# Performance work log

Measured on AMD Instinct MI355X. Metric: run time of the kernel, lower is better.

## Reference

```python
import jax, jax.numpy as jnp
import numpy as np

N, E, FDIM, H = 50000, 1_600_000, 256, 128


def setup_inputs() -> dict:
    key = jax.random.key(0)
    ks = jax.random.split(key, 16)
    s = 0.05
    return {
        "node_features": jax.random.normal(ks[0], (N, FDIM), dtype=jnp.float32),
        "edge_index": jax.random.randint(ks[1], (2, E), 0, N, dtype=jnp.int64),
        # node encoder: Linear(F,H) -> ReLU -> Linear(H,H)
        "enc_w1": jax.random.normal(ks[2], (FDIM, H), dtype=jnp.float32) * s,
        "enc_b1": jnp.zeros((H,), dtype=jnp.float32),
        "enc_w2": jax.random.normal(ks[3], (H, H), dtype=jnp.float32) * s,
        "enc_b2": jnp.zeros((H,), dtype=jnp.float32),
        # three GCNConv layers (weight + bias each)
        "conv_w1": jax.random.normal(ks[4], (H, H), dtype=jnp.float32) * s,
        "conv_b1": jnp.zeros((H,), dtype=jnp.float32),
        "conv_w2": jax.random.normal(ks[5], (H, H), dtype=jnp.float32) * s,
        "conv_b2": jnp.zeros((H,), dtype=jnp.float32),
        "conv_w3": jax.random.normal(ks[6], (H, H), dtype=jnp.float32) * s,
        "conv_b3": jnp.zeros((H,), dtype=jnp.float32),
        # edge classifier: Linear(2H,H) -> ReLU -> Dropout(eval: identity) -> Linear(H,1) -> Sigmoid
        "cls_w1": jax.random.normal(ks[7], (2 * H, H), dtype=jnp.float32) * s,
        "cls_b1": jnp.zeros((H,), dtype=jnp.float32),
        "cls_w2": jax.random.normal(ks[8], (H, 1), dtype=jnp.float32) * s,
        "cls_b2": jnp.zeros((1,), dtype=jnp.float32),
    }


def _gcn_conv(x, w, b, src, dst, norm, n):
    # GCNConv: x' = scatter_add_dst(norm * (x W)[src]) + b  (self-loops already in src/dst/norm)
    xw = x @ w
    out = jax.ops.segment_sum(xw[src] * norm[:, None], dst, num_segments=n)
    return out + b


def reference(node_features, edge_index, enc_w1, enc_b1, enc_w2, enc_b2,
              conv_w1, conv_b1, conv_w2, conv_b2, conv_w3, conv_b3,
              cls_w1, cls_b1, cls_w2, cls_b2):
    n = node_features.shape[0]
    loops = jnp.arange(n, dtype=edge_index.dtype)
    src = jnp.concatenate([edge_index[0], loops])  # (E+N,)
    dst = jnp.concatenate([edge_index[1], loops])
    # symmetric normalization with self-loops (PyG gcn_norm defaults)
    deg = jax.ops.segment_sum(jnp.ones(src.shape, node_features.dtype), dst, num_segments=n)
    dis = jnp.where(deg > 0, jax.lax.rsqrt(jnp.maximum(deg, 1.0)), 0.0)
    norm = dis[src] * dis[dst]  # (E+N,)

    # node encoder
    x = jax.nn.relu(node_features @ enc_w1 + enc_b1) @ enc_w2 + enc_b2
    # stacked GCN layers
    x = jax.nn.relu(_gcn_conv(x, conv_w1, conv_b1, src, dst, norm, n))
    x = jax.nn.relu(_gcn_conv(x, conv_w2, conv_b2, src, dst, norm, n))
    x = _gcn_conv(x, conv_w3, conv_b3, src, dst, norm, n)

    # edge features: gather + concat  -> (E, 2H)
    ef = jnp.concatenate([x[edge_index[0]], x[edge_index[1]]], axis=1)
    h = jax.nn.relu(ef @ cls_w1 + cls_b1)  # Dropout is identity at eval
    scores = jax.nn.sigmoid(h @ cls_w2 + cls_b2)
    return scores.squeeze(-1)  # (E,)
```

## Files before the change

### kernel.cpp

```cpp
#include <hip/hip_runtime.h>
#include <math.h>

#define HDIM 128
#define BSH 7
#define MAXBUCK 512

typedef __attribute__((ext_vector_type(8))) short    bf16x8;
typedef __attribute__((ext_vector_type(4))) float    f32x4;
typedef __attribute__((ext_vector_type(2))) float    f32x2;
typedef __attribute__((ext_vector_type(8))) unsigned short u16x8;
typedef __attribute__((ext_vector_type(4))) unsigned short u16x4;
typedef __attribute__((ext_vector_type(2))) __fp16 f16x2;

__device__ __forceinline__ float bf2f(unsigned short u) {
    union { unsigned int i; float f; } c; c.i = ((unsigned int)u) << 16; return c.f;
}
__device__ __forceinline__ unsigned short f2bf(float f) {
    union { float f; unsigned int i; } c; c.f = f;
    unsigned int r = (c.i + 0x7fffu + ((c.i >> 16) & 1u)) >> 16;
    return (unsigned short)r;
}
__device__ __forceinline__ void f8x8_decp(uint2 v, f32x2* p) {
    p[0] = __builtin_amdgcn_cvt_pk_f32_fp8((int)v.x, false);
    p[1] = __builtin_amdgcn_cvt_pk_f32_fp8((int)v.x, true);
    p[2] = __builtin_amdgcn_cvt_pk_f32_fp8((int)v.y, false);
    p[3] = __builtin_amdgcn_cvt_pk_f32_fp8((int)v.y, true);
}
__device__ __forceinline__ void f8x16_dech(uint4 v, f16x2* h) {
    f32x2 p[8];
    p[0] = __builtin_amdgcn_cvt_pk_f32_fp8((int)v.x, false);
    p[1] = __builtin_amdgcn_cvt_pk_f32_fp8((int)v.x, true);
    p[2] = __builtin_amdgcn_cvt_pk_f32_fp8((int)v.y, false);
    p[3] = __builtin_amdgcn_cvt_pk_f32_fp8((int)v.y, true);
    p[4] = __builtin_amdgcn_cvt_pk_f32_fp8((int)v.z, false);
    p[5] = __builtin_amdgcn_cvt_pk_f32_fp8((int)v.z, true);
    p[6] = __builtin_amdgcn_cvt_pk_f32_fp8((int)v.w, false);
    p[7] = __builtin_amdgcn_cvt_pk_f32_fp8((int)v.w, true);
#pragma unroll
    for (int i = 0; i < 8; i++) h[i] = __builtin_amdgcn_cvt_pkrtz(p[i].x, p[i].y);
}
__device__ __forceinline__ f16x2 pkmax0(f16x2 a) {
    f16x2 r;
    asm("v_pk_max_f16 %0, %1, 0" : "=v"(r) : "v"(a));
    return r;
}
__device__ __forceinline__ float edot16(uint4 pv, const f16x2 (&qh)[8], const f16x2 (&wh)[8]) {
    f16x2 ph[8]; f8x16_dech(pv, ph);
    float acc = 0.f;
#pragma unroll
    for (int i = 0; i < 8; i++)
        acc = __builtin_amdgcn_fdot2(pkmax0(ph[i] + qh[i]), wh[i], acc, false);
    return acc;
}
__device__ __forceinline__ float fsigmoid(float x) {
    float e = __builtin_amdgcn_exp2f(-x * 1.44269504f);
    return __builtin_amdgcn_rcpf(1.f + e);
}

__global__ __launch_bounds__(256) void k_hist(
    const int* __restrict__ dst, int* __restrict__ tot,
    int* __restrict__ hist, int E, int chunk, int nbuck)
{
    __shared__ int h[MAXBUCK];
    for (int i = threadIdx.x; i < MAXBUCK; i += 256) h[i] = 0;
    __syncthreads();
    int beg = blockIdx.x * chunk;
    int fin = min(beg + chunk, E);
    for (int e = beg + threadIdx.x; e < fin; e += 256)
        atomicAdd(&h[dst[e] >> BSH], 1);
    __syncthreads();
    for (int k = threadIdx.x; k < nbuck; k += 256) {
        int v = h[k];
        hist[(size_t)blockIdx.x * nbuck + k] = v;
        if (v) atomicAdd(&tot[k], v);
    }
}

__global__ __launch_bounds__(256) void k_scan_buckets(
    const int* __restrict__ tot, int* __restrict__ gcur, int* __restrict__ base, int nbuck,
    const float* __restrict__ w2src, unsigned short* __restrict__ w2h)
{
    __shared__ int a[MAXBUCK], b[MAXBUCK];
    int t = threadIdx.x;
    if (t < 128) w2h[t] = __builtin_bit_cast(unsigned short, (__fp16)w2src[t]);
    for (int i = t; i < MAXBUCK; i += 256) a[i] = (i < nbuck) ? tot[i] : 0;
    __syncthreads();
    int* s1 = a; int* s2 = b;
    for (int off = 1; off < MAXBUCK; off <<= 1) {
        for (int i = t; i < MAXBUCK; i += 256)
            s2[i] = s1[i] + ((i >= off) ? s1[i - off] : 0);
        __syncthreads();
        int* tmp = s1; s1 = s2; s2 = tmp;
    }
    for (int i = t; i < nbuck; i += 256) {
        int e = (i == 0) ? 0 : s1[i - 1];
        gcur[i] = e;
        base[i] = e;
    }
    if (t == 0) base[nbuck] = s1[nbuck - 1];
}

__global__ __launch_bounds__(256) void k_partition(
    const int* __restrict__ src, const int* __restrict__ dst,
    const int* __restrict__ hist, int* __restrict__ gcur,
    uint2* __restrict__ stag, int E, int chunk, int nbuck)
{
    __shared__ int h[MAXBUCK];
    int t = threadIdx.x;
    for (int k = t; k < nbuck; k += 256) {
        int v = hist[(size_t)blockIdx.x * nbuck + k];
        h[k] = v ? atomicAdd(&gcur[k], v) : 0;
    }
    __syncthreads();
    int beg = blockIdx.x * chunk;
    int fin = min(beg + chunk, E);
    for (int e = beg + t; e < fin; e += 256) {
        unsigned int d = (unsigned int)dst[e];
        unsigned int s = (unsigned int)src[e];
        int pos = atomicAdd(&h[d >> BSH], 1);
        stag[pos] = make_uint2(s | (d << 16), (unsigned int)e);
    }
}

__global__ __launch_bounds__(256) void k_bucket_csr(
    const int* __restrict__ base, const uint2* __restrict__ stag,
    int* __restrict__ row_ptr, int* __restrict__ col, uint2* __restrict__ epk,
    float* __restrict__ dis, int n, int nbuck)
{
    __shared__ int cl[128], sa[128], sb[128], cur[128];
    int k = blockIdx.x;
    int n0 = k << BSH;
    int t = threadIdx.x;
    if (t < 128) cl[t] = 0;
    __syncthreads();
    int b0 = base[k];
    int m = base[k + 1] - b0;
    const uint2* seg = stag + b0;
    for (int i = t; i < m; i += 256) atomicAdd(&cl[(seg[i].x >> 16) & 127], 1);
    __syncthreads();
    int cv = 0;
    if (t < 128) { cv = cl[t]; sa[t] = cv; }
    __syncthreads();
    int* s1 = sa; int* s2 = sb;
    for (int off = 1; off < 128; off <<= 1) {
        if (t < 128) s2[t] = s1[t] + ((t >= off) ? s1[t - off] : 0);
        __syncthreads();
        int* tmp = s1; s1 = s2; s2 = tmp;
    }
    if (t < 128) {
        int node = n0 + t;
        if (node < n) {
            int rpv = b0 + s1[t] - cv;
            row_ptr[node] = rpv;
            cur[t] = rpv;
            dis[node] = rsqrtf(1.0f + (float)cv);
        }
    }
    if (k == 0 && t == 0) row_ptr[n] = base[nbuck];
    __syncthreads();
    for (int i = t; i < m; i += 256) {
        uint2 e = seg[i];
        int pos = atomicAdd(&cur[(e.x >> 16) & 127], 1);
        int s = (int)(e.x & 0xffffu);
        col[pos] = s;
        epk[pos] = make_uint2((unsigned int)s, e.y);
    }
}

struct WEnt { const float* src; unsigned short* dst; int K; };
struct WAll { WEnt w[7]; };

__global__ __launch_bounds__(256) void k_prep_w(WAll all) {
    WEnt e = all.w[blockIdx.y];
    int i = blockIdx.x * 256 + threadIdx.x;
    if (i >= e.K * HDIM) return;
    int k = i >> 7, c = i & 127;
    e.dst[(size_t)c * e.K + k] = f2bf(e.src[i]);
}

__global__ __launch_bounds__(256) void k_gemm_b(
    const unsigned short* __restrict__ X, const unsigned short* __restrict__ Wt,
    const float* __restrict__ bias, const float* __restrict__ scale,
    void* __restrict__ C, int M, int relu_out, int out_mode)
{
    __shared__ unsigned short sW[128 * 128];
    const int t = threadIdx.x;
#pragma unroll
    for (int i = 0; i < 8; i++) {
        int c = t + i * 256;
        int row = c >> 4, o = c & 15;
        int mt = row >> 4, r = row & 15, kc = o >> 2, q = o & 3;
        int lidx = (mt * 4 + kc) * 64 + q * 16 + r;
        *(uint4*)(sW + (size_t)lidx * 8) = *(const uint4*)(Wt + (size_t)c * 8);
    }
    __syncthreads();
    int wave = t >> 6, lane = t & 63;
    int quad = lane >> 4, r = lane & 15;
    int row0 = blockIdx.x * 64 + wave * 16;
    if (row0 >= M) return;
    const unsigned short* xp = X + (size_t)(row0 + r) * 128 + quad * 8;
    f32x4 acc[8];
#pragma unroll
    for (int mt = 0; mt < 8; mt++) acc[mt] = (f32x4){0.f, 0.f, 0.f, 0.f};
#pragma unroll
    for (int kc = 0; kc < 4; kc++) {
        bf16x8 xf = *(const bf16x8*)(xp + kc * 32);
#pragma unroll
        for (int mt = 0; mt < 8; mt++) {
            bf16x8 wf = *(const bf16x8*)(sW + ((size_t)((mt * 4 + kc) * 64 + lane)) * 8);
            acc[mt] = __builtin_amdgcn_mfma_f32_16x16x32_bf16(wf, xf, acc[mt], 0, 0, 0);
        }
    }
    float sc = scale ? scale[row0 + r] : 1.f;
    if (out_mode == 1) {
        unsigned char* cp = (unsigned char*)C + (size_t)(row0 + r) * HDIM + quad * 4;
#pragma unroll
        for (int mt = 0; mt < 8; mt++) {
            float v[4];
#pragma unroll
            for (int j = 0; j < 4; j++) {
                float x = acc[mt][j];
                if (bias) x += bias[mt * 16 + quad * 4 + j];
                if (relu_out) x = fmaxf(x, 0.f);
                v[j] = x * sc;
            }
            int wd = 0;
            wd = __builtin_amdgcn_cvt_pk_fp8_f32(v[0], v[1], wd, false);
            wd = __builtin_amdgcn_cvt_pk_fp8_f32(v[2], v[3], wd, true);
            *(unsigned int*)(cp + mt * 16) = (unsigned int)wd;
        }
    } else {
        unsigned short* cp = (unsigned short*)C + (size_t)(row0 + r) * HDIM + quad * 4;
#pragma unroll
        for (int mt = 0; mt < 8; mt++) {
            u16x4 o;
#pragma unroll
            for (int j = 0; j < 4; j++) {
                float v = acc[mt][j];
                if (bias) v += bias[mt * 16 + quad * 4 + j];
                if (relu_out) v = fmaxf(v, 0.f);
                o[j] = f2bf(v * sc);
            }
            *(u16x4*)(cp + mt * 16) = o;
        }
    }
}

__global__ __launch_bounds__(256) void k_gemm_nf(
    const float* __restrict__ X, const unsigned short* __restrict__ Wt,
    const float* __restrict__ bias, unsigned short* __restrict__ C,
    int M, int relu_out)
{
    const int K = 256;
    __shared__ unsigned short sW[128 * 256];
    const int t = threadIdx.x;
#pragma unroll
    for (int i = 0; i < 16; i++) {
        int c = t + i * 256;
        int row = c >> 5, o = c & 31;
        int mt = row >> 4, r = row & 15, kc = o >> 2, q = o & 3;
        int lidx = (mt * 8 + kc) * 64 + q * 16 + r;
        *(uint4*)(sW + (size_t)lidx * 8) = *(const uint4*)(Wt + (size_t)c * 8);
    }
    __syncthreads();
    int wave = t >> 6, lane = t & 63;
    int quad = lane >> 4, r = lane & 15;
    int row0 = blockIdx.x * 64 + wave * 16;
    if (row0 >= M) return;
    const float* xp = X + (size_t)(row0 + r) * K + quad * 8;
    f32x4 acc[8];
#pragma unroll
    for (int mt = 0; mt < 8; mt++) acc[mt] = (f32x4){0.f, 0.f, 0.f, 0.f};
#pragma unroll 2
    for (int kc = 0; kc < 8; kc++) {
        float4 xa = *(const float4*)(xp + kc * 32);
        float4 xb = *(const float4*)(xp + kc * 32 + 4);
        bf16x8 xf;
        xf[0] = (short)f2bf(xa.x); xf[1] = (short)f2bf(xa.y);
        xf[2] = (short)f2bf(xa.z); xf[3] = (short)f2bf(xa.w);
        xf[4] = (short)f2bf(xb.x); xf[5] = (short)f2bf(xb.y);
        xf[6] = (short)f2bf(xb.z); xf[7] = (short)f2bf(xb.w);
#pragma unroll
        for (int mt = 0; mt < 8; mt++) {
            bf16x8 wf = *(const bf16x8*)(sW + ((size_t)((mt * 8 + kc) * 64 + lane)) * 8);
            acc[mt] = __builtin_amdgcn_mfma_f32_16x16x32_bf16(wf, xf, acc[mt], 0, 0, 0);
        }
    }
    unsigned short* cp = C + (size_t)(row0 + r) * HDIM + quad * 4;
#pragma unroll
    for (int mt = 0; mt < 8; mt++) {
        u16x4 o;
#pragma unroll
        for (int j = 0; j < 4; j++) {
            float v = acc[mt][j];
            if (bias) v += bias[mt * 16 + quad * 4 + j];
            if (relu_out) v = fmaxf(v, 0.f);
            o[j] = f2bf(v);
        }
        *(u16x4*)(cp + mt * 16) = o;
    }
}

__global__ __launch_bounds__(256) void k_aggregate_f8(
    const int* __restrict__ row_ptr, const int* __restrict__ col,
    const float* __restrict__ dis, const uint2* __restrict__ y8,
    const float* __restrict__ bias, unsigned short* __restrict__ out, int n, int relu_out)
{
    int wid = (blockIdx.x * 256 + threadIdx.x) >> 6;
    if (wid >= n) return;
    int lane = threadIdx.x & 63;
    int q = lane >> 4, t = lane & 15;
    f32x2 acc[4];
    {
        uint2 sv = y8[(size_t)wid * 16 + t];
        f32x2 p[4]; f8x8_decp(sv, p);
#pragma unroll
        for (int i = 0; i < 4; i++) acc[i] = (q == 0) ? p[i] : (f32x2){0.f, 0.f};
    }
    int beg = row_ptr[wid], end = row_ptr[wid + 1];
    int j = beg + q;
    for (; j + 28 < end; j += 32) {
        int s[8];
        uint2 v[8];
#pragma unroll
        for (int u = 0; u < 8; u++) s[u] = col[j + u * 4];
#pragma unroll
        for (int u = 0; u < 8; u++) v[u] = y8[(size_t)s[u] * 16 + t];
#pragma unroll
        for (int u = 0; u < 8; u++) {
            f32x2 p[4]; f8x8_decp(v[u], p);
#pragma unroll
            for (int i = 0; i < 4; i++) acc[i] += p[i];
        }
    }
    for (; j + 12 < end; j += 16) {
        int s0 = col[j], s1 = col[j + 4], s2 = col[j + 8], s3 = col[j + 12];
        uint2 v0 = y8[(size_t)s0 * 16 + t];
        uint2 v1 = y8[(size_t)s1 * 16 + t];
        uint2 v2 = y8[(size_t)s2 * 16 + t];
        uint2 v3 = y8[(size_t)s3 * 16 + t];
        f32x2 p0[4], p1[4], p2[4], p3[4];
        f8x8_decp(v0, p0); f8x8_decp(v1, p1); f8x8_decp(v2, p2); f8x8_decp(v3, p3);
#pragma unroll
        for (int i = 0; i < 4; i++) acc[i] += (p0[i] + p1[i]) + (p2[i] + p3[i]);
    }
    for (; j < end; j += 4) {
        int s = col[j];
        uint2 v = y8[(size_t)s * 16 + t];
        f32x2 p[4]; f8x8_decp(v, p);
#pragma unroll
        for (int i = 0; i < 4; i++) acc[i] += p[i];
    }
#pragma unroll
    for (int i = 0; i < 4; i++) {
        acc[i].x += __shfl_xor(acc[i].x, 16, 64);
        acc[i].y += __shfl_xor(acc[i].y, 16, 64);
        acc[i].x += __shfl_xor(acc[i].x, 32, 64);
        acc[i].y += __shfl_xor(acc[i].y, 32, 64);
    }
    if (q == 0) {
        float di = dis[wid];
        u16x8 o;
#pragma unroll
        for (int i = 0; i < 4; i++) {
            float v0 = di * acc[i].x + bias[t * 8 + i * 2];
            float v1 = di * acc[i].y + bias[t * 8 + i * 2 + 1];
            if (relu_out) { v0 = fmaxf(v0, 0.f); v1 = fmaxf(v1, 0.f); }
            o[i * 2]     = f2bf(v0);
            o[i * 2 + 1] = f2bf(v1);
        }
        *(u16x8*)(out + (size_t)wid * HDIM + t * 8) = o;
    }
}

__global__ __launch_bounds__(256) void k_edge_score_csr(
    const int* __restrict__ row_ptr, const uint2* __restrict__ epk,
    const uint4* __restrict__ P8, const uint4* __restrict__ Q8,
    const unsigned short* __restrict__ w2h, const float* __restrict__ b2,
    float* __restrict__ out, int n)
{
    int wid = (blockIdx.x * 256 + threadIdx.x) >> 6;
    if (wid >= n) return;
    int lane = threadIdx.x & 63;
    unsigned g = (unsigned)(lane >> 3), t = (unsigned)(lane & 7);
    f16x2 wh[8], qh[8];
    {
        uint4 wv0 = *(const uint4*)(w2h + t * 16);
        uint4 wv1 = *(const uint4*)(w2h + t * 16 + 8);
        wh[0] = __builtin_bit_cast(f16x2, wv0.x);
        wh[1] = __builtin_bit_cast(f16x2, wv0.y);
        wh[2] = __builtin_bit_cast(f16x2, wv0.z);
        wh[3] = __builtin_bit_cast(f16x2, wv0.w);
        wh[4] = __builtin_bit_cast(f16x2, wv1.x);
        wh[5] = __builtin_bit_cast(f16x2, wv1.y);
        wh[6] = __builtin_bit_cast(f16x2, wv1.z);
        wh[7] = __builtin_bit_cast(f16x2, wv1.w);
        uint4 qv = Q8[(unsigned)wid * 8u + t];
        f8x16_dech(qv, qh);
    }
    float bb = b2[0];
    int beg = row_ptr[wid], end = row_ptr[wid + 1];
    int j = beg + (int)g;
    for (; j + 8 < end; j += 16) {
        uint2 e0 = epk[j], e1 = epk[j + 8];
        uint4 p0 = P8[e0.x * 8u + t];
        uint4 p1 = P8[e1.x * 8u + t];
        float s0 = edot16(p0, qh, wh);
        float s1 = edot16(p1, qh, wh);
        s0 += __shfl_xor(s0, 4, 8); s1 += __shfl_xor(s1, 4, 8);
        s0 += __shfl_xor(s0, 2, 8); s1 += __shfl_xor(s1, 2, 8);
        s0 += __shfl_xor(s0, 1, 8); s1 += __shfl_xor(s1, 1, 8);
        float sv = (t == 0) ? s0 : s1;
        unsigned eid = (t == 0) ? e0.y : e1.y;
        if (t < 2)
            __builtin_nontemporal_store(fsigmoid(sv + bb), &out[eid]);
    }
    if (j < end) {
        uint2 e0 = epk[j];
        uint4 p0 = P8[e0.x * 8u + t];
        float s0 = edot16(p0, qh, wh);
        s0 += __shfl_xor(s0, 4, 8);
        s0 += __shfl_xor(s0, 2, 8);
        s0 += __shfl_xor(s0, 1, 8);
        if (t == 0)
            __builtin_nontemporal_store(fsigmoid(s0 + bb), &out[e0.y]);
    }
}

extern "C" void kernel_launch(void* const* d_in, const int* in_sizes, int n_in,
                              void* d_out, int out_size, void* d_ws, size_t ws_size,
                              hipStream_t stream) {
    const float* nf   = (const float*)d_in[0];
    const int*   ei   = (const int*)d_in[1];
    const float* ew1  = (const float*)d_in[2];
    const float* eb1  = (const float*)d_in[3];
    const float* ew2  = (const float*)d_in[4];
    const float* eb2  = (const float*)d_in[5];
    const float* cw1  = (const float*)d_in[6];
    const float* cb1  = (const float*)d_in[7];
    const float* cw2  = (const float*)d_in[8];
    const float* cb2  = (const float*)d_in[9];
    const float* cw3  = (const float*)d_in[10];
    const float* cb3  = (const float*)d_in[11];
    const float* clw1 = (const float*)d_in[12];
    const float* clb1 = (const float*)d_in[13];
    const float* clw2 = (const float*)d_in[14];
    const float* clb2 = (const float*)d_in[15];
    float* out = (float*)d_out;

    const int FD = 256;
    const int N = in_sizes[0] / FD;
    const int E = in_sizes[1] / 2;
    const int NBUCK = (N + 127) >> BSH;
    const int PBLK = 256;
    const int chunk = (E + PBLK - 1) / PBLK;

    size_t Np = ((size_t)N + 256) & ~(size_t)255;
    char* w = (char*)d_ws;
    float* dis     = (float*)w;            w += Np * 4;
    int*   tot     = (int*)w;              w += MAXBUCK * 4;
    int*   gcur    = (int*)w;              w += MAXBUCK * 4;
    int*   base    = (int*)w;              w += (MAXBUCK + 4) * 4;
    int*   hist    = (int*)w;              w += (size_t)PBLK * MAXBUCK * 4;
    int*   row_ptr = (int*)w;              w += Np * 4;
    uint2* stag    = (uint2*)w;            w += (size_t)E * 8;
    uint2* epk     = (uint2*)w;            w += (size_t)E * 8;
    int*   col     = (int*)w;              w += (((size_t)E * 4) + 255) & ~(size_t)255;
    unsigned short* bufA = (unsigned short*)w;  w += (size_t)N * HDIM * 2;
    unsigned short* bufB = (unsigned short*)w;  w += (size_t)N * HDIM * 2;
    unsigned short* bufC = (unsigned short*)w;  w += (size_t)N * HDIM * 2;
    unsigned char*  f8X  = (unsigned char*)w;   w += ((size_t)N * HDIM + 255) & ~(size_t)255;
    unsigned char*  f8P  = (unsigned char*)w;   w += ((size_t)N * HDIM + 255) & ~(size_t)255;
    unsigned char*  f8Q  = (unsigned char*)w;   w += ((size_t)N * HDIM + 255) & ~(size_t)255;
    unsigned short* wtE1 = (unsigned short*)w;  w += 256 * HDIM * 2;
    unsigned short* wtE2 = (unsigned short*)w;  w += 128 * HDIM * 2;
    unsigned short* wtC1 = (unsigned short*)w;  w += 128 * HDIM * 2;
    unsigned short* wtC2 = (unsigned short*)w;  w += 128 * HDIM * 2;
    unsigned short* wtC3 = (unsigned short*)w;  w += 128 * HDIM * 2;
    unsigned short* wtT  = (unsigned short*)w;  w += 128 * HDIM * 2;
    unsigned short* wtB  = (unsigned short*)w;  w += 128 * HDIM * 2;
    unsigned short* w2h  = (unsigned short*)w;  w += 256 * 2;

    int gemm_grid = (N + 63) / 64;
    int ag = (N + 3) / 4;

    WAll wa;
    wa.w[0] = { ew1,               wtE1, 256 };
    wa.w[1] = { ew2,               wtE2, 128 };
    wa.w[2] = { cw1,               wtC1, 128 };
    wa.w[3] = { cw2,               wtC2, 128 };
    wa.w[4] = { cw3,               wtC3, 128 };
    wa.w[5] = { clw1,              wtT,  128 };
    wa.w[6] = { clw1 + 128 * HDIM, wtB,  128 };
    k_prep_w<<<dim3(128, 7), 256, 0, stream>>>(wa);

    hipMemsetAsync(tot, 0, MAXBUCK * sizeof(int), stream);
    k_hist<<<PBLK, 256, 0, stream>>>(ei + E, tot, hist, E, chunk, NBUCK);
    k_scan_buckets<<<1, 256, 0, stream>>>(tot, gcur, base, NBUCK, clw2, w2h);
    k_partition<<<PBLK, 256, 0, stream>>>(ei, ei + E, hist, gcur, stag, E, chunk, NBUCK);
    k_bucket_csr<<<NBUCK, 256, 0, stream>>>(base, stag, row_ptr, col, epk, dis, N, NBUCK);

    k_gemm_nf<<<gemm_grid, 256, 0, stream>>>(nf, wtE1, eb1, bufA, N, 1);
    k_gemm_b<<<gemm_grid, 256, 0, stream>>>(bufA, wtE2, eb2, nullptr, bufB, N, 0, 0);

    k_gemm_b<<<gemm_grid, 256, 0, stream>>>(bufB, wtC1, nullptr, dis, f8X, N, 0, 1);
    k_aggregate_f8<<<ag, 256, 0, stream>>>(row_ptr, col, dis, (const uint2*)f8X, cb1, bufC, N, 1);
    k_gemm_b<<<gemm_grid, 256, 0, stream>>>(bufC, wtC2, nullptr, dis, f8X, N, 0, 1);
    k_aggregate_f8<<<ag, 256, 0, stream>>>(row_ptr, col, dis, (const uint2*)f8X, cb2, bufA, N, 1);
    k_gemm_b<<<gemm_grid, 256, 0, stream>>>(bufA, wtC3, nullptr, dis, f8X, N, 0, 1);
    k_aggregate_f8<<<ag, 256, 0, stream>>>(row_ptr, col, dis, (const uint2*)f8X, cb3, bufB, N, 0);

    k_gemm_b<<<gemm_grid, 256, 0, stream>>>(bufB, wtT, clb1, nullptr, f8P, N, 0, 1);
    k_gemm_b<<<gemm_grid, 256, 0, stream>>>(bufB, wtB, nullptr, nullptr, f8Q, N, 0, 1);

    k_edge_score_csr<<<ag, 256, 0, stream>>>(row_ptr, epk, (const uint4*)f8P, (const uint4*)f8Q,
                                             w2h, clb2, out, N);
}
```

Measured before the change: 446.9 us.

## Fold encoder second linear into first conv weight; fuse P/Q GEMMs; nontemporal index loads

Precomputes We2·Wc1 and be2·Wc1 on device so the encoder's second linear layer and the first GCN projection run as one GEMM, removing one full N×H pass. The two classifier projection GEMMs are merged into one kernel that reads the input tile once and writes both fp8 outputs. Column and edge index loads in the aggregation and edge-scoring kernels become nontemporal to reduce cache pollution. The fold changes rounding, since the product is formed in fp32 and then stored in bf16, and the fused kernel uses twice the LDS per block.

```diff
diff --git a/kernel.cpp b/kernel.cpp
--- a/kernel.cpp
+++ b/kernel.cpp
@@ -56,6 +56,10 @@
     float e = __builtin_amdgcn_exp2f(-x * 1.44269504f);
     return __builtin_amdgcn_rcpf(1.f + e);
 }
+__device__ __forceinline__ uint2 nt_load_u2(const uint2* p) {
+    unsigned long long v = __builtin_nontemporal_load((const unsigned long long*)p);
+    return make_uint2((unsigned)v, (unsigned)(v >> 32));
+}
 
 __global__ __launch_bounds__(256) void k_hist(
     const int* __restrict__ dst, int* __restrict__ tot,
@@ -168,7 +172,7 @@
 }
 
 struct WEnt { const float* src; unsigned short* dst; int K; };
-struct WAll { WEnt w[7]; };
+struct WAll { WEnt w[5]; };
 
 __global__ __launch_bounds__(256) void k_prep_w(WAll all) {
     WEnt e = all.w[blockIdx.y];
@@ -176,6 +180,24 @@
     if (i >= e.K * HDIM) return;
     int k = i >> 7, c = i & 127;
     e.dst[(size_t)c * e.K + k] = f2bf(e.src[i]);
+}
+
+__global__ __launch_bounds__(256) void k_fold(
+    const float* __restrict__ We2, const float* __restrict__ be2,
+    const float* __restrict__ Wc1, unsigned short* __restrict__ WtF,
+    float* __restrict__ bF)
+{
+    int i = blockIdx.x * 256 + threadIdx.x;
+    int c = i >> 7, k = i & 127;
+    float s = 0.f;
+    for (int j = 0; j < 128; j++)
+        s += We2[k * 128 + j] * Wc1[j * 128 + c];
+    WtF[(size_t)c * 128 + k] = f2bf(s);
+    if (i < 128) {
+        float b = 0.f;
+        for (int j = 0; j < 128; j++) b += be2[j] * Wc1[j * 128 + i];
+        bF[i] = b;
+    }
 }
 
 __global__ __launch_bounds__(256) void k_gemm_b(
@@ -246,6 +268,63 @@
     }
 }
 
+__global__ __launch_bounds__(256) void k_gemm_pq(
+    const unsigned short* __restrict__ X, const unsigned short* __restrict__ WtP,
+    const unsigned short* __restrict__ WtQ, const float* __restrict__ biasP,
+    unsigned char* __restrict__ P, unsigned char* __restrict__ Q, int M)
+{
+    __shared__ unsigned short sW[2 * 128 * 128];
+    const int t = threadIdx.x;
+#pragma unroll
+    for (int i = 0; i < 8; i++) {
+        int c = t + i * 256;
+        int row = c >> 4, o = c & 15;
+        int mt = row >> 4, r = row & 15, kc = o >> 2, q = o & 3;
+        int lidx = (mt * 4 + kc) * 64 + q * 16 + r;
+        *(uint4*)(sW + (size_t)lidx * 8)         = *(const uint4*)(WtP + (size_t)c * 8);
+        *(uint4*)(sW + 16384 + (size_t)lidx * 8) = *(const uint4*)(WtQ + (size_t)c * 8);
+    }
+    __syncthreads();
+    int wave = t >> 6, lane = t & 63;
+    int quad = lane >> 4, r = lane & 15;
+    int row0 = blockIdx.x * 64 + wave * 16;
+    if (row0 >= M) return;
+    const unsigned short* xp = X + (size_t)(row0 + r) * 128 + quad * 8;
+    f32x4 accP[8], accQ[8];
+#pragma unroll
+    for (int mt = 0; mt < 8; mt++) {
+        accP[mt] = (f32x4){0.f, 0.f, 0.f, 0.f};
+        accQ[mt] = (f32x4){0.f, 0.f, 0.f, 0.f};
+    }
+#pragma unroll
+    for (int kc = 0; kc < 4; kc++) {
+        bf16x8 xf = *(const bf16x8*)(xp + kc * 32);
+#pragma unroll
+        for (int mt = 0; mt < 8; mt++) {
+            bf16x8 wfp = *(const bf16x8*)(sW + ((size_t)((mt * 4 + kc) * 64 + lane)) * 8);
+            bf16x8 wfq = *(const bf16x8*)(sW + 16384 + ((size_t)((mt * 4 + kc) * 64 + lane)) * 8);
+            accP[mt] = __builtin_amdgcn_mfma_f32_16x16x32_bf16(wfp, xf, accP[mt], 0, 0, 0);
+            accQ[mt] = __builtin_amdgcn_mfma_f32_16x16x32_bf16(wfq, xf, accQ[mt], 0, 0, 0);
+        }
+    }
+    unsigned char* pp = P + (size_t)(row0 + r) * HDIM + quad * 4;
+    unsigned char* qp = Q + (size_t)(row0 + r) * HDIM + quad * 4;
+#pragma unroll
+    for (int mt = 0; mt < 8; mt++) {
+        int wdp = 0, wdq = 0;
+        float p0 = accP[mt][0] + biasP[mt * 16 + quad * 4 + 0];
+        float p1 = accP[mt][1] + biasP[mt * 16 + quad * 4 + 1];
+        float p2 = accP[mt][2] + biasP[mt * 16 + quad * 4 + 2];
+        float p3 = accP[mt][3] + biasP[mt * 16 + quad * 4 + 3];
+        wdp = __builtin_amdgcn_cvt_pk_fp8_f32(p0, p1, wdp, false);
+        wdp = __builtin_amdgcn_cvt_pk_fp8_f32(p2, p3, wdp, true);
+        wdq = __builtin_amdgcn_cvt_pk_fp8_f32(accQ[mt][0], accQ[mt][1], wdq, false);
+        wdq = __builtin_amdgcn_cvt_pk_fp8_f32(accQ[mt][2], accQ[mt][3], wdq, true);
+        *(unsigned int*)(pp + mt * 16) = (unsigned int)wdp;
+        *(unsigned int*)(qp + mt * 16) = (unsigned int)wdq;
+    }
+}
+
 __global__ __launch_bounds__(256) void k_gemm_nf(
     const float* __restrict__ X, const unsigned short* __restrict__ Wt,
     const float* __restrict__ bias, unsigned short* __restrict__ C,
@@ -323,7 +402,7 @@
         int s[8];
         uint2 v[8];
 #pragma unroll
-        for (int u = 0; u < 8; u++) s[u] = col[j + u * 4];
+        for (int u = 0; u < 8; u++) s[u] = __builtin_nontemporal_load(&col[j + u * 4]);
 #pragma unroll
         for (int u = 0; u < 8; u++) v[u] = y8[(size_t)s[u] * 16 + t];
 #pragma unroll
@@ -334,7 +413,10 @@
         }
     }
     for (; j + 12 < end; j += 16) {
-        int s0 = col[j], s1 = col[j + 4], s2 = col[j + 8], s3 = col[j + 12];
+        int s0 = __builtin_nontemporal_load(&col[j]);
+        int s1 = __builtin_nontemporal_load(&col[j + 4]);
+        int s2 = __builtin_nontemporal_load(&col[j + 8]);
+        int s3 = __builtin_nontemporal_load(&col[j + 12]);
         uint2 v0 = y8[(size_t)s0 * 16 + t];
         uint2 v1 = y8[(size_t)s1 * 16 + t];
         uint2 v2 = y8[(size_t)s2 * 16 + t];
@@ -345,7 +427,7 @@
         for (int i = 0; i < 4; i++) acc[i] += (p0[i] + p1[i]) + (p2[i] + p3[i]);
     }
     for (; j < end; j += 4) {
-        int s = col[j];
+        int s = __builtin_nontemporal_load(&col[j]);
         uint2 v = y8[(size_t)s * 16 + t];
         f32x2 p[4]; f8x8_decp(v, p);
 #pragma unroll
@@ -402,7 +484,8 @@
     int beg = row_ptr[wid], end = row_ptr[wid + 1];
     int j = beg + (int)g;
     for (; j + 8 < end; j += 16) {
-        uint2 e0 = epk[j], e1 = epk[j + 8];
+        uint2 e0 = nt_load_u2(&epk[j]);
+        uint2 e1 = nt_load_u2(&epk[j + 8]);
         uint4 p0 = P8[e0.x * 8u + t];
         uint4 p1 = P8[e1.x * 8u + t];
         float s0 = edot16(p0, qh, wh);
@@ -416,7 +499,7 @@
             __builtin_nontemporal_store(fsigmoid(sv + bb), &out[eid]);
     }
     if (j < end) {
-        uint2 e0 = epk[j];
+        uint2 e0 = nt_load_u2(&epk[j]);
         uint4 p0 = P8[e0.x * 8u + t];
         float s0 = edot16(p0, qh, wh);
         s0 += __shfl_xor(s0, 4, 8);
@@ -473,26 +556,25 @@
     unsigned char*  f8P  = (unsigned char*)w;   w += ((size_t)N * HDIM + 255) & ~(size_t)255;
     unsigned char*  f8Q  = (unsigned char*)w;   w += ((size_t)N * HDIM + 255) & ~(size_t)255;
     unsigned short* wtE1 = (unsigned short*)w;  w += 256 * HDIM * 2;
-    unsigned short* wtE2 = (unsigned short*)w;  w += 128 * HDIM * 2;
-    unsigned short* wtC1 = (unsigned short*)w;  w += 128 * HDIM * 2;
+    unsigned short* wtF  = (unsigned short*)w;  w += 128 * HDIM * 2;
     unsigned short* wtC2 = (unsigned short*)w;  w += 128 * HDIM * 2;
     unsigned short* wtC3 = (unsigned short*)w;  w += 128 * HDIM * 2;
     unsigned short* wtT  = (unsigned short*)w;  w += 128 * HDIM * 2;
     unsigned short* wtB  = (unsigned short*)w;  w += 128 * HDIM * 2;
     unsigned short* w2h  = (unsigned short*)w;  w += 256 * 2;
+    float*          bF   = (float*)w;           w += 128 * 4;
 
     int gemm_grid = (N + 63) / 64;
     int ag = (N + 3) / 4;
 
     WAll wa;
     wa.w[0] = { ew1,               wtE1, 256 };
-    wa.w[1] = { ew2,               wtE2, 128 };
-    wa.w[2] = { cw1,               wtC1, 128 };
-    wa.w[3] = { cw2,               wtC2, 128 };
-    wa.w[4] = { cw3,               wtC3, 128 };
-    wa.w[5] = { clw1,              wtT,  128 };
-    wa.w[6] = { clw1 + 128 * HDIM, wtB,  128 };
-    k_prep_w<<<dim3(128, 7), 256, 0, stream>>>(wa);
+    wa.w[1] = { cw2,               wtC2, 128 };
+    wa.w[2] = { cw3,               wtC3, 128 };
+    wa.w[3] = { clw1,              wtT,  128 };
+    wa.w[4] = { clw1 + 128 * HDIM, wtB,  128 };
+    k_prep_w<<<dim3(128, 5), 256, 0, stream>>>(wa);
+    k_fold<<<64, 256, 0, stream>>>(ew2, eb2, cw1, wtF, bF);
 
     hipMemsetAsync(tot, 0, MAXBUCK * sizeof(int), stream);
     k_hist<<<PBLK, 256, 0, stream>>>(ei + E, tot, hist, E, chunk, NBUCK);
@@ -501,17 +583,15 @@
     k_bucket_csr<<<NBUCK, 256, 0, stream>>>(base, stag, row_ptr, col, epk, dis, N, NBUCK);
 
     k_gemm_nf<<<gemm_grid, 256, 0, stream>>>(nf, wtE1, eb1, bufA, N, 1);
-    k_gemm_b<<<gemm_grid, 256, 0, stream>>>(bufA, wtE2, eb2, nullptr, bufB, N, 0, 0);
-
-    k_gemm_b<<<gemm_grid, 256, 0, stream>>>(bufB, wtC1, nullptr, dis, f8X, N, 0, 1);
+
+    k_gemm_b<<<gemm_grid, 256, 0, stream>>>(bufA, wtF, bF, dis, f8X, N, 0, 1);
     k_aggregate_f8<<<ag, 256, 0, stream>>>(row_ptr, col, dis, (const uint2*)f8X, cb1, bufC, N, 1);
     k_gemm_b<<<gemm_grid, 256, 0, stream>>>(bufC, wtC2, nullptr, dis, f8X, N, 0, 1);
     k_aggregate_f8<<<ag, 256, 0, stream>>>(row_ptr, col, dis, (const uint2*)f8X, cb2, bufA, N, 1);
     k_gemm_b<<<gemm_grid, 256, 0, stream>>>(bufA, wtC3, nullptr, dis, f8X, N, 0, 1);
     k_aggregate_f8<<<ag, 256, 0, stream>>>(row_ptr, col, dis, (const uint2*)f8X, cb3, bufB, N, 0);
 
-    k_gemm_b<<<gemm_grid, 256, 0, stream>>>(bufB, wtT, clb1, nullptr, f8P, N, 0, 1);
-    k_gemm_b<<<gemm_grid, 256, 0, stream>>>(bufB, wtB, nullptr, nullptr, f8Q, N, 0, 1);
+    k_gemm_pq<<<gemm_grid, 256, 0, stream>>>(bufB, wtT, wtB, clb1, f8P, f8Q, N);
 
     k_edge_score_csr<<<ag, 256, 0, stream>>>(row_ptr, epk, (const uint4*)f8P, (const uint4*)f8Q,
                                              w2h, clb2, out, N);
```

Result: slower. 475.6 us (+6.4%).
